# Optimization experiments

Hardware: AMD Instinct MI355X
Metric: run time of the kernel (lower is better)

The kernel has to match this reference:

```python
import jax, jax.numpy as jnp
import numpy as np

N_PTS = 2_097_152


def _pe(x):
    # num_frequencies = 3: [sin(pi x), cos(pi x), sin(2pi x), cos(2pi x), sin(4pi x), cos(4pi x)] -> [N,18]
    parts = []
    for i in range(3):
        f = np.float32((2.0 ** i) * np.pi)
        parts.append(jnp.sin(f * x))
        parts.append(jnp.cos(f * x))
    return jnp.concatenate(parts, axis=-1)


def _trilinear(vol, coords):
    # vol: [C,D,H,W]; coords: [N,3] in grid_sample order (x->W, y->H, z->D),
    # align_corners=False, zeros padding. Returns [C,N].
    C, D, H, W = vol.shape
    x = (coords[:, 0] + 1.0) * (W * 0.5) - 0.5
    y = (coords[:, 1] + 1.0) * (H * 0.5) - 0.5
    z = (coords[:, 2] + 1.0) * (D * 0.5) - 0.5
    x0f = jnp.floor(x); y0f = jnp.floor(y); z0f = jnp.floor(z)
    tx = x - x0f; ty = y - y0f; tz = z - z0f
    x0 = x0f.astype(jnp.int32); y0 = y0f.astype(jnp.int32); z0 = z0f.astype(jnp.int32)

    def corner(zi, yi, xi, w):
        valid = (zi >= 0) & (zi < D) & (yi >= 0) & (yi < H) & (xi >= 0) & (xi < W)
        v = vol[:, jnp.clip(zi, 0, D - 1), jnp.clip(yi, 0, H - 1), jnp.clip(xi, 0, W - 1)]
        return v * (w * valid)[None, :]

    return (corner(z0, y0, x0, (1 - tz) * (1 - ty) * (1 - tx))
            + corner(z0, y0, x0 + 1, (1 - tz) * (1 - ty) * tx)
            + corner(z0, y0 + 1, x0, (1 - tz) * ty * (1 - tx))
            + corner(z0, y0 + 1, x0 + 1, (1 - tz) * ty * tx)
            + corner(z0 + 1, y0, x0, tz * (1 - ty) * (1 - tx))
            + corner(z0 + 1, y0, x0 + 1, tz * (1 - ty) * tx)
            + corner(z0 + 1, y0 + 1, x0, tz * ty * (1 - tx))
            + corner(z0 + 1, y0 + 1, x0 + 1, tz * ty * tx))


def setup_inputs() -> dict:
    key = jax.random.key(0)
    ks = jax.random.split(key, 11)
    q = 1.0
    inp = {
        'x': jax.random.uniform(ks[0], (N_PTS, 3), dtype=jnp.float32),
        'grid0': jax.random.normal(ks[1], (4, 32, 32, 32), dtype=jnp.float32),
        'grid1': jax.random.normal(ks[2], (4, 64, 64, 64), dtype=jnp.float32),
        'grid2': jax.random.normal(ks[3], (2, 128, 128, 128), dtype=jnp.float32),
        'noise0': jax.random.uniform(ks[4], (4, 32, 32, 32), dtype=jnp.float32) / q - 0.5 / q,
        'noise1': jax.random.uniform(ks[5], (4, 64, 64, 64), dtype=jnp.float32) / q - 0.5 / q,
        'noise2': jax.random.uniform(ks[6], (2, 128, 128, 128), dtype=jnp.float32) / q - 0.5 / q,
        'w1': jax.random.normal(ks[7], (64, 20), dtype=jnp.float32) * (1.0 / np.sqrt(20.0)),
        'b1': jnp.zeros((64,), dtype=jnp.float32),
        'w2': jax.random.normal(ks[8], (7, 64), dtype=jnp.float32) * (1.0 / np.sqrt(64.0)),
        'b2': jnp.zeros((7,), dtype=jnp.float32),
    }
    return inp


def reference(x, grid0, grid1, grid2, noise0, noise1, noise2, w1, b1, w2, b2):
    pe = _pe(x)  # [N,18]
    feats = []
    for i, (g, nz) in enumerate(((grid0, noise0), (grid1, noise1), (grid2, noise2))):
        gv = g + nz  # training-mode noise injection, shared across the two samples
        feats.append(_trilinear(gv, pe[:, i * 6:i * 6 + 3]))
        feats.append(_trilinear(gv, pe[:, i * 6 + 3:i * 6 + 6]))
    f = jnp.concatenate(feats, axis=0).T  # [N,20]
    h = jax.nn.leaky_relu(f @ w1.T + b1, negative_slope=0.01)
    return h @ w2.T + b2  # [N,7]
```

## Files before the change

### kernel.cpp

```cpp
#include <hip/hip_runtime.h>


#define NB 4096
#define KB 128
#define NXCD 8

typedef _Float16 f16x2 __attribute__((ext_vector_type(2)));
typedef __fp16  h8    __attribute__((ext_vector_type(8)));
typedef float   f4    __attribute__((ext_vector_type(4)));

__device__ __forceinline__ f16x2 pkrtz(float a, float b) {
    return __builtin_bit_cast(f16x2, __builtin_amdgcn_cvt_pkrtz(a, b));
}
__device__ __forceinline__ unsigned pkrtzu(float a, float b) {
    return __builtin_bit_cast(unsigned, __builtin_amdgcn_cvt_pkrtz(a, b));
}
__device__ __forceinline__ float fdot2(f16x2 a, f16x2 b, float c) {
    return __builtin_amdgcn_fdot2(a, b, c, false);
}
__device__ __forceinline__ f16x2 u2h(unsigned u) { return __builtin_bit_cast(f16x2, u); }

__device__ __forceinline__ int bin_of(float xv, float yv, float zv) {
    int qx = min(max((int)(xv * 16.f), 0), 15);
    int qy = min(max((int)(yv * 16.f), 0), 15);
    int qz = min(max((int)(zv * 16.f), 0), 15);
    return (qz << 8) | (qy << 4) | qx;
}

#define PREP_BLOCKS 9568

__global__ __launch_bounds__(256)
void prep_k(const float* __restrict__ x,
            const float* __restrict__ g0, const float* __restrict__ n0,
            const float* __restrict__ g1, const float* __restrict__ n1,
            const float* __restrict__ g2, const float* __restrict__ n2,
            const float* __restrict__ w1, const float* __restrict__ w2,
            uint2* __restrict__ p0, uint2* __restrict__ p1,
            unsigned* __restrict__ p2,
            unsigned short* __restrict__ w1p, unsigned short* __restrict__ w2p,
            int* __restrict__ counts, int npts) {
    __shared__ int h[NB];
    const int b = blockIdx.x, t = threadIdx.x;
    if (b < 8256) {
        int i = b * 256 + t;
        if (i < 2113536) {
            int z = i / 16512, rem = i % 16512;
            int y = rem / 129, xp = rem % 129;
            int v = (z * 128 + y) * 128 + max(xp - 1, 0);
            p2[i] = pkrtzu(g2[v] + n2[v], g2[2097152 + v] + n2[2097152 + v]);
        }
    } else if (b < 9296) {
        int i = (b - 8256) * 256 + t;
        if (i < 266240) {
            int z = i / 4160, rem = i % 4160;
            int y = rem / 65, xp = rem % 65;
            int v = (z * 64 + y) * 64 + max(xp - 1, 0);
            uint2 r;
            r.x = pkrtzu(g1[v] + n1[v], g1[262144 + v] + n1[262144 + v]);
            r.y = pkrtzu(g1[524288 + v] + n1[524288 + v], g1[786432 + v] + n1[786432 + v]);
            p1[i] = r;
        }
    } else if (b < 9428) {
        int i = (b - 9296) * 256 + t;
        if (i < 33792) {
            int z = i / 1056, rem = i % 1056;
            int y = rem / 33, xp = rem % 33;
            int v = (z * 32 + y) * 32 + max(xp - 1, 0);
            uint2 r;
            r.x = pkrtzu(g0[v] + n0[v], g0[32768 + v] + n0[32768 + v]);
            r.y = pkrtzu(g0[65536 + v] + n0[65536 + v], g0[98304 + v] + n0[98304 + v]);
            p0[i] = r;
        }
    } else if (b < 9556) {
        const int cb = b - 9428;
        for (int i = t; i < NB; i += 256) h[i] = 0;
        __syncthreads();
        const int chunk = (npts + KB - 1) / KB;
        const int s = cb * chunk, e = min(s + chunk, npts);
        for (int p = s + t; p < e; p += 256)
            atomicAdd(&h[bin_of(x[3 * p], x[3 * p + 1], x[3 * p + 2])], 1);
        __syncthreads();
        for (int i = t; i < NB; i += 256) counts[cb * NB + i] = h[i];
    } else {
        int i = (b - 9556) * 256 + t;
        if (i < 2048) {
            int j = i >> 5, k = i & 31;
            float v = (k < 20) ? w1[j * 20 + k] : 0.f;
            w1p[i] = __builtin_bit_cast(unsigned short, (_Float16)v);
        } else if (i < 3072) {
            int i2 = i - 2048;
            int o = i2 >> 6, jj = i2 & 63;
            float v = (o < 7) ? w2[o * 64 + jj] : 0.f;
            w2p[i2] = __builtin_bit_cast(unsigned short, (_Float16)v);
        }
    }
}

__global__ __launch_bounds__(256)
void scan_rows_k(const int* __restrict__ counts, int* __restrict__ offs,
                 int* __restrict__ rowsum) {
    __shared__ int tile[KB][32];
    const int g = blockIdx.x, t = threadIdx.x;
    for (int idx = t; idx < KB * 32; idx += 256) {
        int b = idx >> 5, j = idx & 31;
        tile[b][j] = counts[b * NB + g * 32 + j];
    }
    __syncthreads();
    if (t < 32) {
        int run = 0;
#pragma unroll 8
        for (int b = 0; b < KB; ++b) {
            int v = tile[b][t];
            tile[b][t] = run;
            run += v;
        }
        rowsum[g * 32 + t] = run;
    }
    __syncthreads();
    for (int idx = t; idx < KB * 32; idx += 256) {
        int b = idx >> 5, j = idx & 31;
        offs[b * NB + g * 32 + j] = tile[b][j];
    }
}

__global__ __launch_bounds__(1024)
void scatter_k(const float* __restrict__ x, const int* __restrict__ offs,
               const int* __restrict__ rowsum, float4* __restrict__ sorted,
               int npts) {
    __shared__ int base[NB];
    __shared__ int sh[1024];
    const int t = threadIdx.x, b = blockIdx.x;

    int t4 = t * 4;
    int v0 = rowsum[t4], v1 = rowsum[t4 + 1], v2 = rowsum[t4 + 2], v3 = rowsum[t4 + 3];
    int s4 = v0 + v1 + v2 + v3;
    sh[t] = s4;
    __syncthreads();
    for (int d = 1; d < 1024; d <<= 1) {
        int add = (t >= d) ? sh[t - d] : 0;
        __syncthreads();
        sh[t] += add;
        __syncthreads();
    }
    int run = sh[t] - s4;
    base[t4] = run; run += v0;
    base[t4 + 1] = run; run += v1;
    base[t4 + 2] = run; run += v2;
    base[t4 + 3] = run;
    __syncthreads();
    for (int i = t; i < NB; i += 1024) base[i] += offs[b * NB + i];
    __syncthreads();

    const int chunk = (npts + KB - 1) / KB;
    const int s = b * chunk, e = min(s + chunk, npts);
    for (int p = s + t; p < e; p += 1024) {
        float xv = x[3 * p], yv = x[3 * p + 1], zv = x[3 * p + 2];
        int pos = atomicAdd(&base[bin_of(xv, yv, zv)], 1);
        float4 v; v.x = xv; v.y = yv; v.z = zv; v.w = __int_as_float(p);
        sorted[pos] = v;
    }
}

template<int S>
__device__ __forceinline__ void tl_setup(float cx, float cy, float cz,
        int& o00, int& o01, int& o10, int& o11,
        f16x2& w00, f16x2& w01, f16x2& w10, f16x2& w11) {
    const float hs = (float)S * 0.5f;
    float gx = fmaf(cx, hs, hs - 0.5f);
    float gy = fmaf(cy, hs, hs - 0.5f);
    float gz = fmaf(cz, hs, hs - 0.5f);
    float fx = floorf(gx), fy = floorf(gy), fz = floorf(gz);
    float tx = gx - fx, ty = gy - fy, tz = gz - fz;
    int x0 = (int)fx, y0 = (int)fy, z0 = (int)fz;
    float wx0 = (1.f - tx) * ((x0 >= 0)    ? 1.f : 0.f);
    float wx1 = tx         * ((x0 + 1 < S) ? 1.f : 0.f);
    float wy0 = (1.f - ty) * ((y0 >= 0)    ? 1.f : 0.f);
    float wy1 = ty         * ((y0 + 1 < S) ? 1.f : 0.f);
    float wz0 = (1.f - tz) * ((z0 >= 0)    ? 1.f : 0.f);
    float wz1 = tz         * ((z0 + 1 < S) ? 1.f : 0.f);
    const int xb = x0 + 1;
    f16x2 wx2 = pkrtz(wx0, wx1);
    int ys0 = max(y0, 0), ys1 = min(y0 + 1, S - 1);
    int zs0 = max(z0, 0), zs1 = min(z0 + 1, S - 1);
    o00 = (zs0 * S + ys0) * (S + 1) + xb;
    o01 = (zs0 * S + ys1) * (S + 1) + xb;
    o10 = (zs1 * S + ys0) * (S + 1) + xb;
    o11 = (zs1 * S + ys1) * (S + 1) + xb;
    float a00 = wz0 * wy0, a01 = wz0 * wy1, a10 = wz1 * wy0, a11 = wz1 * wy1;
    w00 = pkrtz(a00, a00) * wx2;
    w01 = pkrtz(a01, a01) * wx2;
    w10 = pkrtz(a10, a10) * wx2;
    w11 = pkrtz(a11, a11) * wx2;
}

struct TL4S {
    uint4 r00, r01, r10, r11;
    f16x2 w00, w01, w10, w11;
};
template<int S>
__device__ __forceinline__ TL4S tl4_issue(const uint2* __restrict__ vol,
                                          float cx, float cy, float cz) {
    TL4S r; int o00, o01, o10, o11;
    tl_setup<S>(cx, cy, cz, o00, o01, o10, o11, r.w00, r.w01, r.w10, r.w11);
    r.r00 = *reinterpret_cast<const uint4*>(vol + o00);
    r.r01 = *reinterpret_cast<const uint4*>(vol + o01);
    r.r10 = *reinterpret_cast<const uint4*>(vol + o10);
    r.r11 = *reinterpret_cast<const uint4*>(vol + o11);
    return r;
}
#define TL4_ROW(s, R, WP, f) { uint4 r = (s).R; \
    unsigned pc0 = __builtin_amdgcn_perm(r.z, r.x, 0x05040100u); \
    unsigned pc1 = __builtin_amdgcn_perm(r.z, r.x, 0x07060302u); \
    unsigned pc2 = __builtin_amdgcn_perm(r.w, r.y, 0x05040100u); \
    unsigned pc3 = __builtin_amdgcn_perm(r.w, r.y, 0x07060302u); \
    (f)[0] = fdot2((s).WP, u2h(pc0), (f)[0]); (f)[1] = fdot2((s).WP, u2h(pc1), (f)[1]); \
    (f)[2] = fdot2((s).WP, u2h(pc2), (f)[2]); (f)[3] = fdot2((s).WP, u2h(pc3), (f)[3]); }
__device__ __forceinline__ void tl4_consume(const TL4S& s, float* f) {
    TL4_ROW(s, r00, w00, f) TL4_ROW(s, r01, w01, f)
    TL4_ROW(s, r10, w10, f) TL4_ROW(s, r11, w11, f)
}

struct TL2S {
    uint2 r00, r01, r10, r11;
    f16x2 w00, w01, w10, w11;
};
template<int S>
__device__ __forceinline__ TL2S tl2_issue(const unsigned* __restrict__ vol,
                                          float cx, float cy, float cz) {
    TL2S r; int o00, o01, o10, o11;
    tl_setup<S>(cx, cy, cz, o00, o01, o10, o11, r.w00, r.w01, r.w10, r.w11);
    r.r00 = *reinterpret_cast<const uint2*>(vol + o00);
    r.r01 = *reinterpret_cast<const uint2*>(vol + o01);
    r.r10 = *reinterpret_cast<const uint2*>(vol + o10);
    r.r11 = *reinterpret_cast<const uint2*>(vol + o11);
    return r;
}
#define TL2_ROW(s, R, WP, f) { uint2 r = (s).R; \
    unsigned pc0 = __builtin_amdgcn_perm(r.y, r.x, 0x05040100u); \
    unsigned pc1 = __builtin_amdgcn_perm(r.y, r.x, 0x07060302u); \
    (f)[0] = fdot2((s).WP, u2h(pc0), (f)[0]); (f)[1] = fdot2((s).WP, u2h(pc1), (f)[1]); }
__device__ __forceinline__ void tl2_consume(const TL2S& s, float* f) {
    TL2_ROW(s, r00, w00, f) TL2_ROW(s, r01, w01, f)
    TL2_ROW(s, r10, w10, f) TL2_ROW(s, r11, w11, f)
}

__device__ __forceinline__ void trig3(float x, float y, float z,
        float* s1, float* c1, float* s2, float* c2, float* s4, float* c4) {
    const float v[3] = {x, y, z};
#pragma unroll
    for (int d = 0; d < 3; ++d) {
        float sa = __builtin_amdgcn_sinf(0.5f * v[d]);
        float ca = __builtin_amdgcn_cosf(0.5f * v[d]);
        s1[d] = sa; c1[d] = ca;
        float sb = 2.f * sa * ca, cb = fmaf(-2.f * sa, sa, 1.f);
        s2[d] = sb; c2[d] = cb;
        s4[d] = 2.f * sb * cb; c4[d] = fmaf(-2.f * sb, sb, 1.f);
    }
}

__global__ __launch_bounds__(256, 3)
void motion_grid_main(const float4* __restrict__ sorted,
                      const float* __restrict__ xraw,
                      const uint2* __restrict__ g0v,
                      const uint2* __restrict__ g1v,
                      const unsigned* __restrict__ g2v,
                      const unsigned short* __restrict__ w1p_,
                      const unsigned short* __restrict__ w2p_,
                      const float* __restrict__ b1,
                      const float* __restrict__ b2,
                      float* __restrict__ out, int npts, int sortedMode,
                      int nblk) {
    __shared__ __align__(16) char smem[4 * 7424];
    int bid = blockIdx.x;
    if ((nblk & (NXCD - 1)) == 0) {
        int cpx = nblk / NXCD;
        bid = (bid % NXCD) * cpx + bid / NXCD;
    }
    const int tid = threadIdx.x;
    const int w = tid >> 6, l = tid & 63, c = l & 15, g = l >> 4;
    char* wbase = smem + w * 7424;
    const int p = bid * 256 + tid;

    float xv = 0.f, yv = 0.f, zv = 0.f;
    int orig = -1;
    if (p < npts) {
        if (sortedMode) {
            float4 sp = sorted[p];
            xv = sp.x; yv = sp.y; zv = sp.z; orig = __float_as_int(sp.w);
        } else {
            xv = xraw[3 * p]; yv = xraw[3 * p + 1]; zv = xraw[3 * p + 2];
            orig = p;
        }
    }
    float s1[3], c1[3], s2[3], c2[3], s4[3], c4[3];
    trig3(xv, yv, zv, s1, c1, s2, c2, s4, c4);

    TL4S S0s = tl4_issue<32>(g0v, s1[0], s1[1], s1[2]);
    TL4S S0c = tl4_issue<32>(g0v, c1[0], c1[1], c1[2]);
    TL4S S1s = tl4_issue<64>(g1v, s2[0], s2[1], s2[2]);
    TL4S S1c = tl4_issue<64>(g1v, c2[0], c2[1], c2[2]);
    TL2S S2s = tl2_issue<128>(g2v, s4[0], s4[1], s4[2]);
    TL2S S2c = tl2_issue<128>(g2v, c4[0], c4[1], c4[2]);

    float f[20];
#pragma unroll
    for (int i = 0; i < 20; ++i) f[i] = 0.f;
    tl4_consume(S0s, f + 0);  tl4_consume(S0c, f + 4);
    tl4_consume(S1s, f + 8);  tl4_consume(S1c, f + 12);
    tl2_consume(S2s, f + 16); tl2_consume(S2c, f + 18);
    {
        uint4* fs = (uint4*)(wbase + l * 80);
        fs[0] = make_uint4(pkrtzu(f[0], f[1]), pkrtzu(f[2], f[3]),
                           pkrtzu(f[4], f[5]), pkrtzu(f[6], f[7]));
        fs[1] = make_uint4(pkrtzu(f[8], f[9]), pkrtzu(f[10], f[11]),
                           pkrtzu(f[12], f[13]), pkrtzu(f[14], f[15]));
        fs[2] = make_uint4(pkrtzu(f[16], f[17]), pkrtzu(f[18], f[19]), 0u, 0u);
        fs[3] = make_uint4(0u, 0u, 0u, 0u);
    }

    h8 a1f0 = *(const h8*)(w1p_ + (0 * 16 + c) * 32 + g * 8);
    h8 a1f1 = *(const h8*)(w1p_ + (1 * 16 + c) * 32 + g * 8);
    h8 a1f2 = *(const h8*)(w1p_ + (2 * 16 + c) * 32 + g * 8);
    h8 a1f3 = *(const h8*)(w1p_ + (3 * 16 + c) * 32 + g * 8);
    f4 b1f0 = *(const f4*)(b1 + 0 * 16 + g * 4);
    f4 b1f1 = *(const f4*)(b1 + 1 * 16 + g * 4);
    f4 b1f2 = *(const f4*)(b1 + 2 * 16 + g * 4);
    f4 b1f3 = *(const f4*)(b1 + 3 * 16 + g * 4);
    h8 a20 = *(const h8*)(w2p_ + c * 64 + g * 8);
    h8 a21 = *(const h8*)(w2p_ + c * 64 + 32 + g * 8);
    float b2f0 = (g * 4 + 0 < 7) ? b2[g * 4 + 0] : 0.f;
    float b2f1 = (g * 4 + 1 < 7) ? b2[g * 4 + 1] : 0.f;
    float b2f2 = (g * 4 + 2 < 7) ? b2[g * 4 + 2] : 0.f;
    float b2f3 = (g * 4 + 3 < 7) ? b2[g * 4 + 3] : 0.f;

    const f4 zero4 = {0.f, 0.f, 0.f, 0.f};
#pragma unroll
    for (int n = 0; n < 4; ++n) {
        h8 bn = *(const h8*)(wbase + (n * 16 + c) * 80 + g * 16);
        __builtin_amdgcn_s_setprio(1);
        f4 d0 = __builtin_amdgcn_mfma_f32_16x16x32_f16(a1f0, bn, zero4, 0, 0, 0);
        f4 d1 = __builtin_amdgcn_mfma_f32_16x16x32_f16(a1f1, bn, zero4, 0, 0, 0);
        f4 d2m = __builtin_amdgcn_mfma_f32_16x16x32_f16(a1f2, bn, zero4, 0, 0, 0);
        f4 d3 = __builtin_amdgcn_mfma_f32_16x16x32_f16(a1f3, bn, zero4, 0, 0, 0);
        __builtin_amdgcn_s_setprio(0);
        d0 += b1f0; d1 += b1f1; d2m += b1f2; d3 += b1f3;
        {
            float h0 = fmaxf(d0[0], 0.01f * d0[0]), h1 = fmaxf(d0[1], 0.01f * d0[1]);
            float h2 = fmaxf(d0[2], 0.01f * d0[2]), h3 = fmaxf(d0[3], 0.01f * d0[3]);
            *(uint2*)(wbase + 5120 + c * 144 + 0 * 32 + g * 8) =
                make_uint2(pkrtzu(h0, h1), pkrtzu(h2, h3));
            h0 = fmaxf(d1[0], 0.01f * d1[0]); h1 = fmaxf(d1[1], 0.01f * d1[1]);
            h2 = fmaxf(d1[2], 0.01f * d1[2]); h3 = fmaxf(d1[3], 0.01f * d1[3]);
            *(uint2*)(wbase + 5120 + c * 144 + 1 * 32 + g * 8) =
                make_uint2(pkrtzu(h0, h1), pkrtzu(h2, h3));
            h0 = fmaxf(d2m[0], 0.01f * d2m[0]); h1 = fmaxf(d2m[1], 0.01f * d2m[1]);
            h2 = fmaxf(d2m[2], 0.01f * d2m[2]); h3 = fmaxf(d2m[3], 0.01f * d2m[3]);
            *(uint2*)(wbase + 5120 + c * 144 + 2 * 32 + g * 8) =
                make_uint2(pkrtzu(h0, h1), pkrtzu(h2, h3));
            h0 = fmaxf(d3[0], 0.01f * d3[0]); h1 = fmaxf(d3[1], 0.01f * d3[1]);
            h2 = fmaxf(d3[2], 0.01f * d3[2]); h3 = fmaxf(d3[3], 0.01f * d3[3]);
            *(uint2*)(wbase + 5120 + c * 144 + 3 * 32 + g * 8) =
                make_uint2(pkrtzu(h0, h1), pkrtzu(h2, h3));
        }
        h8 hb0 = *(const h8*)(wbase + 5120 + c * 144 + g * 16);
        h8 hb1 = *(const h8*)(wbase + 5120 + c * 144 + 64 + g * 16);
        __builtin_amdgcn_s_setprio(1);
        f4 o2 = __builtin_amdgcn_mfma_f32_16x16x32_f16(a20, hb0, zero4, 0, 0, 0);
        o2 = __builtin_amdgcn_mfma_f32_16x16x32_f16(a21, hb1, o2, 0, 0, 0);
        __builtin_amdgcn_s_setprio(0);
        int og = __shfl(orig, n * 16 + c, 64);
        if (og >= 0 && g < 2) {
            float* op = out + (size_t)og * 7 + g * 4;
            op[0] = o2[0] + b2f0;
            op[1] = o2[1] + b2f1;
            op[2] = o2[2] + b2f2;
            if (g == 0) op[3] = o2[3] + b2f3;
        }
    }
}

extern "C" void kernel_launch(void* const* d_in, const int* in_sizes, int n_in,
                              void* d_out, int out_size, void* d_ws, size_t ws_size,
                              hipStream_t stream) {
    const float* x  = (const float*)d_in[0];
    const float* g0 = (const float*)d_in[1];
    const float* g1 = (const float*)d_in[2];
    const float* g2 = (const float*)d_in[3];
    const float* n0 = (const float*)d_in[4];
    const float* n1 = (const float*)d_in[5];
    const float* n2 = (const float*)d_in[6];
    const float* w1 = (const float*)d_in[7];
    const float* b1 = (const float*)d_in[8];
    const float* w2 = (const float*)d_in[9];
    const float* b2 = (const float*)d_in[10];
    float* out = (float*)d_out;

    const int npts = in_sizes[0] / 3;

    char* ws = (char*)d_ws;
    size_t cur = 0;
    auto alloc = [&](size_t bytes) {
        char* p = ws + cur;
        cur = (cur + bytes + 255) & ~(size_t)255;
        return p;
    };
    uint2*          p0       = (uint2*)         alloc(33792u   * 8 + 64);
    uint2*          p1       = (uint2*)         alloc(266240u  * 8 + 64);
    unsigned*       p2       = (unsigned*)      alloc(2113536u * 4 + 64);
    unsigned short* w1p      = (unsigned short*)alloc(2048 * 2);
    unsigned short* w2p      = (unsigned short*)alloc(1024 * 2);
    int*            counts   = (int*)           alloc((size_t)KB * NB * 4);
    int*            offs     = (int*)           alloc((size_t)KB * NB * 4);
    int*            rowsum   = (int*)           alloc(NB * 4);
    float4*         sorted   = (float4*)        alloc((size_t)npts * 16);
    const int useSorted = (ws_size >= cur) ? 1 : 0;

    prep_k<<<PREP_BLOCKS, 256, 0, stream>>>(x, g0, n0, g1, n1, g2, n2, w1, w2,
                                            p0, p1, p2, w1p, w2p, counts, npts);
    if (useSorted) {
        scan_rows_k<<<NB / 32, 256, 0, stream>>>(counts, offs, rowsum);
        scatter_k<<<KB, 1024, 0, stream>>>(x, offs, rowsum, sorted, npts);
    }

    const int nblk = (npts + 255) / 256;
    motion_grid_main<<<nblk, 256, 0, stream>>>(
        sorted, x, p0, p1, p2, w1p, w2p, b1, b2, out, npts, useSorted, nblk);
}
```

Measured before the change: 211.8 us.

## Refine spatial binning to 16384 bins with packed 16-bit shared histograms

Raises the spatial sort from 16x16x16 to 16x32x32 bins so points processed together are closer in space, which should improve cache locality of the trilinear gathers in the main kernel. To keep the histogram within shared memory, counts are packed as two 16-bit counters per 32-bit word, updated with shifted atomic adds. The scatter prefix scan now handles 16 bins per thread. In exchange the count, offset and scan arrays grow fourfold, adding memory traffic to the scan and scatter stages, and the scan_rows kernel (not shown) must also cope with the larger NB.

```diff
diff --git a/kernel.cpp b/kernel.cpp
--- a/kernel.cpp
+++ b/kernel.cpp
@@ -1,7 +1,7 @@
 #include <hip/hip_runtime.h>
 
 
-#define NB 4096
+#define NB 16384
 #define KB 128
 #define NXCD 8
 
@@ -22,9 +22,9 @@
 
 __device__ __forceinline__ int bin_of(float xv, float yv, float zv) {
     int qx = min(max((int)(xv * 16.f), 0), 15);
-    int qy = min(max((int)(yv * 16.f), 0), 15);
-    int qz = min(max((int)(zv * 16.f), 0), 15);
-    return (qz << 8) | (qy << 4) | qx;
+    int qy = min(max((int)(yv * 32.f), 0), 31);
+    int qz = min(max((int)(zv * 32.f), 0), 31);
+    return (qz << 9) | (qy << 4) | qx;
 }
 
 #define PREP_BLOCKS 9568
@@ -39,7 +39,7 @@
             unsigned* __restrict__ p2,
             unsigned short* __restrict__ w1p, unsigned short* __restrict__ w2p,
             int* __restrict__ counts, int npts) {
-    __shared__ int h[NB];
+    __shared__ unsigned h32[NB / 2];
     const int b = blockIdx.x, t = threadIdx.x;
     if (b < 8256) {
         int i = b * 256 + t;
@@ -73,14 +73,17 @@
         }
     } else if (b < 9556) {
         const int cb = b - 9428;
-        for (int i = t; i < NB; i += 256) h[i] = 0;
+        for (int i = t; i < NB / 2; i += 256) h32[i] = 0u;
         __syncthreads();
         const int chunk = (npts + KB - 1) / KB;
         const int s = cb * chunk, e = min(s + chunk, npts);
-        for (int p = s + t; p < e; p += 256)
-            atomicAdd(&h[bin_of(x[3 * p], x[3 * p + 1], x[3 * p + 2])], 1);
+        for (int p = s + t; p < e; p += 256) {
+            int bin = bin_of(x[3 * p], x[3 * p + 1], x[3 * p + 2]);
+            atomicAdd(&h32[bin >> 1], 1u << ((bin & 1) * 16));
+        }
         __syncthreads();
-        for (int i = t; i < NB; i += 256) counts[cb * NB + i] = h[i];
+        for (int i = t; i < NB; i += 256)
+            counts[cb * NB + i] = (int)((h32[i >> 1] >> ((i & 1) * 16)) & 0xffffu);
     } else {
         int i = (b - 9556) * 256 + t;
         if (i < 2048) {
@@ -131,10 +134,9 @@
     __shared__ int sh[1024];
     const int t = threadIdx.x, b = blockIdx.x;
 
-    int t4 = t * 4;
-    int v0 = rowsum[t4], v1 = rowsum[t4 + 1], v2 = rowsum[t4 + 2], v3 = rowsum[t4 + 3];
-    int s4 = v0 + v1 + v2 + v3;
-    sh[t] = s4;
+    int s16 = 0;
+    for (int i = 0; i < 16; ++i) s16 += rowsum[t * 16 + i];
+    sh[t] = s16;
     __syncthreads();
     for (int d = 1; d < 1024; d <<= 1) {
         int add = (t >= d) ? sh[t - d] : 0;
@@ -142,11 +144,12 @@
         sh[t] += add;
         __syncthreads();
     }
-    int run = sh[t] - s4;
-    base[t4] = run; run += v0;
-    base[t4 + 1] = run; run += v1;
-    base[t4 + 2] = run; run += v2;
-    base[t4 + 3] = run;
+    int run = sh[t] - s16;
+    for (int i = 0; i < 16; ++i) {
+        int v = rowsum[t * 16 + i];
+        base[t * 16 + i] = run;
+        run += v;
+    }
     __syncthreads();
     for (int i = t; i < NB; i += 1024) base[i] += offs[b * NB + i];
     __syncthreads();
```

New measurement: 198.8 us. 6.1% less time.
